# Performance work log

Measured on AMD Instinct MI355X. Metric: run time of the kernel, lower is better.

## Reference

```python
import jax, jax.numpy as jnp
import numpy as np

N_NODES = 100000


def _gcn_norm(edge_index, num_nodes):
    # PyG gcn_norm with add_self_loops=True, edge_weight=1:
    # A_hat = A + I; norm_e = deg^{-1/2}[src] * deg^{-1/2}[dst]
    loop = jnp.arange(num_nodes, dtype=edge_index.dtype)
    src = jnp.concatenate([edge_index[0], loop])
    dst = jnp.concatenate([edge_index[1], loop])
    deg = jax.ops.segment_sum(jnp.ones_like(src, dtype=jnp.float32), dst,
                              num_segments=num_nodes)
    dinv = jnp.where(deg > 0, jax.lax.rsqrt(deg), 0.0)
    norm = dinv[src] * dinv[dst]  # [E + N]
    return src, dst, norm


def _gcn_conv(x, src, dst, norm, W, b, num_nodes):
    h = x @ W                                  # [N, out] dense GEMM
    msg = h[src] * norm[:, None]               # gather + scale per edge
    out = jax.ops.segment_sum(msg, dst, num_segments=num_nodes)
    return out + b


def setup_inputs() -> dict:
    key = jax.random.key(0)
    k1, k2, k3, k4, k5, k6 = jax.random.split(key, 6)
    in_c, hid_c, out_c = 128, 128, 64
    E = 3200000
    x = jax.random.normal(k1, (N_NODES, in_c), dtype=jnp.float32)
    edge_index = jax.random.randint(k2, (2, E), 0, N_NODES, dtype=jnp.int64)
    # Glorot-style init for GCNConv linear weights, zero bias (PyG default)
    W1 = jax.random.normal(k3, (in_c, hid_c), dtype=jnp.float32) / np.sqrt(in_c)
    b1 = jnp.zeros((hid_c,), dtype=jnp.float32)
    W2 = jax.random.normal(k4, (hid_c, out_c), dtype=jnp.float32) / np.sqrt(hid_c)
    b2 = jnp.zeros((out_c,), dtype=jnp.float32)
    return {"x": x, "edge_index": edge_index, "W1": W1, "b1": b1,
            "W2": W2, "b2": b2}


def reference(x, edge_index, W1, b1, W2, b2):
    # Dropout is identity in eval mode (F.dropout(training=False)).
    src, dst, norm = _gcn_norm(edge_index, N_NODES)
    h = _gcn_conv(x, src, dst, norm, W1, b1, N_NODES)
    out = _gcn_conv(h, src, dst, norm, W2, b2, N_NODES)
    return out
```

## Files before the change

### kernel.cpp

```cpp
#include <hip/hip_runtime.h>
#include <hip/hip_fp16.h>
#include <cstdint>
#include <cstddef>


#define NB    391
#define BSH   8
#define CAPS  32
#define PBLK  512
#define OVB   64
#define CAPB  9216

typedef _Float16 half8 __attribute__((ext_vector_type(8)));
typedef float    floatx4 __attribute__((ext_vector_type(4)));
typedef unsigned uint4v  __attribute__((ext_vector_type(4)));


__global__ __launch_bounds__(256) void partition_k(
    const int* __restrict__ src, const int* __restrict__ dst,
    unsigned long long* __restrict__ ov64, int* __restrict__ ovcnt,
    unsigned* __restrict__ tailbuf, int* __restrict__ tailcnt, int E) {
    __shared__ unsigned stag[NB][CAPS + 1];
    __shared__ int scnt[NB];
    __shared__ int ovn;
    const int t = threadIdx.x, bid = blockIdx.x;
    for (int i = t; i < NB; i += 256) scnt[i] = 0;
    if (t == 0) ovn = 0;
    __syncthreads();

    const int Q = E >> 2;
    const int per = (Q + PBLK - 1) / PBLK;
    const int qbeg = bid * per;
    const int qend = min(qbeg + per, Q);
    const int4* src4 = (const int4*)src;
    const int4* dst4 = (const int4*)dst;

    for (int q = qbeg + t; q < qend; q += 256) {
        const int4 s4 = src4[q];
        const int4 d4 = dst4[q];
#pragma unroll
        for (int j = 0; j < 4; ++j) {
            const int s = (&s4.x)[j], d = (&d4.x)[j];
            const int b = d >> BSH;
            const unsigned rec = ((unsigned)(d & 255) << 17) | (unsigned)s;
            const int slot = atomicAdd(&scnt[b], 1);
            if (slot < CAPS) stag[b][slot] = rec;
            else {
                const int pos = atomicAdd(&ovn, 1);
                if (pos < OVB)
                    ov64[(size_t)bid * OVB + pos] =
                        ((unsigned long long)(unsigned)d << 17) | (unsigned)s;
            }
        }
    }
    if (bid == 0) {
        for (int e = (E & ~3) + t; e < E; e += 256) {
            const int s = src[e], d = dst[e];
            const int b = d >> BSH;
            const unsigned rec = ((unsigned)(d & 255) << 17) | (unsigned)s;
            const int slot = atomicAdd(&scnt[b], 1);
            if (slot < CAPS) stag[b][slot] = rec;
            else {
                const int pos = atomicAdd(&ovn, 1);
                if (pos < OVB)
                    ov64[(size_t)bid * OVB + pos] =
                        ((unsigned long long)(unsigned)d << 17) | (unsigned)s;
            }
        }
    }
    __syncthreads();

    for (int i = t; i < NB * CAPS; i += 256) {
        const int b = i >> 5, j = i & 31;
        if (j < min(scnt[b], CAPS))
            tailbuf[((size_t)b * PBLK + bid) * CAPS + j] = stag[b][j];
    }
    for (int b = t; b < NB; b += 256)
        tailcnt[bid * NB + b] = min(scnt[b], CAPS);
    if (t == 0) ovcnt[bid] = min(ovn, OVB);
}

__global__ __launch_bounds__(256) void build_w12_k(
    const unsigned long long* __restrict__ ov64, const int* __restrict__ ovcnt,
    const unsigned* __restrict__ tailbuf, const int* __restrict__ tailcnt,
    int* __restrict__ rbeg, int* __restrict__ rend,
    int* __restrict__ csr, float* __restrict__ dinv,
    const float* __restrict__ W1, const float* __restrict__ W2,
    const float* __restrict__ b1, _Float16* __restrict__ BhiT,
    _Float16* __restrict__ BloT, float* __restrict__ c2, int N) {
    __shared__ int tcs[PBLK];
    __shared__ int soff[PBLK];
    __shared__ int sseg[256];
    __shared__ unsigned lrec[CAPB + 64];
    __shared__ int cnt[256];
    __shared__ int scan[256];
    __shared__ int lpos[256];
    __shared__ int tcum_sh;
    __shared__ int ovn_sh;
    const int t = threadIdx.x, b = blockIdx.x;

    if (b >= NB) {
        const int bb = b - NB;
        if (bb < 32) {
            const int r = bb * 4 + (t >> 6);
            const int c = t & 63;
            float acc = 0.f;
            for (int k = 0; k < 128; ++k) acc += W1[r * 128 + k] * W2[k * 64 + c];
            const _Float16 h = (_Float16)acc;
            BhiT[c * 128 + r] = h;
            BloT[c * 128 + r] = (_Float16)(acc - (float)h);
        } else if (t < 64) {
            float acc = 0.f;
            for (int k = 0; k < 128; ++k) acc += b1[k] * W2[k * 64 + t];
            c2[t] = acc;
        }
        return;
    }

    const int n0 = b << BSH;
    const int nn = min(256, N - n0);
    const int gbase = b * CAPB;
    const size_t tb0 = (size_t)b * PBLK * CAPS;

    for (int i = t; i < PBLK; i += 256) tcs[i] = tailcnt[i * NB + b];
    cnt[t] = 0;
    if (t == 0) ovn_sh = 0;
    __syncthreads();

    const int a0 = tcs[2 * t], a1 = tcs[2 * t + 1];
    sseg[t] = a0 + a1;
    __syncthreads();
    for (int o = 1; o < 256; o <<= 1) {
        int x = (t >= o) ? sseg[t - o] : 0;
        __syncthreads(); sseg[t] += x; __syncthreads();
    }
    const int ex2 = sseg[t] - (a0 + a1);
    soff[2 * t] = ex2;
    soff[2 * t + 1] = ex2 + a0;
    if (t == 255) tcum_sh = sseg[255];
    __syncthreads();
    const int tcum = tcum_sh;

    for (int i = t; i < PBLK * CAPS; i += 256) {
        const int seg = i >> 5, j = i & 31;
        if (j < tcs[seg]) lrec[soff[seg] + j] = tailbuf[tb0 + i];
    }
    for (int blk = t; blk < PBLK; blk += 256) {
        const int c = ovcnt[blk];
        for (int i2 = 0; i2 < c; ++i2) {
            const unsigned long long r = ov64[(size_t)blk * OVB + i2];
            const int dd = (int)(r >> 17);
            if ((dd >> BSH) == b) {
                const int pos = atomicAdd(&ovn_sh, 1);
                lrec[tcum + pos] =
                    ((unsigned)(dd & 255) << 17) | (unsigned)(r & 0x1FFFFu);
            }
        }
    }
    __syncthreads();

    const int tot = tcum + ovn_sh;
    for (int i = t; i < tot; i += 256) atomicAdd(&cnt[lrec[i] >> 17], 1);
    __syncthreads();

    scan[t] = cnt[t];
    __syncthreads();
    for (int o = 1; o < 256; o <<= 1) {
        int x = (t >= o) ? scan[t - o] : 0;
        __syncthreads(); scan[t] += x; __syncthreads();
    }
    const int excl = scan[t] - cnt[t];
    lpos[t] = excl;
    if (t < nn) {
        rbeg[n0 + t] = gbase + excl;
        rend[n0 + t] = gbase + scan[t];
        dinv[n0 + t] = rsqrtf((float)(cnt[t] + 1));
    }
    __syncthreads();

    for (int i = t; i < tot; i += 256) {
        const unsigned r = lrec[i];
        const int pq = atomicAdd(&lpos[r >> 17], 1);
        csr[gbase + pq] = (int)(r & 0x1FFFFu);
    }
}

__global__ __launch_bounds__(256) void gemm_mfma_k(
    const float* __restrict__ X, const _Float16* __restrict__ BhiT,
    const _Float16* __restrict__ BloT, const float* __restrict__ dinv,
    __half* __restrict__ g, int N) {
    const int t = threadIdx.x;
    const int wave = t >> 6, lane = t & 63;
    const int m16 = lane & 15;
    const int quad = lane >> 4;
    const int rowbase = blockIdx.x * 64 + wave * 16;
    const int arow = min(rowbase + m16, N - 1);

    floatx4 acc[4] = {{0.f,0.f,0.f,0.f},{0.f,0.f,0.f,0.f},
                      {0.f,0.f,0.f,0.f},{0.f,0.f,0.f,0.f}};

#pragma unroll
    for (int ks = 0; ks < 4; ++ks) {
        const int k0 = ks * 32 + quad * 8;
        const float4 xa = *(const float4*)(X + (size_t)arow * 128 + k0);
        const float4 xb = *(const float4*)(X + (size_t)arow * 128 + k0 + 4);
        const float xs[8] = {xa.x, xa.y, xa.z, xa.w, xb.x, xb.y, xb.z, xb.w};
        half8 ahi, alo;
#pragma unroll
        for (int j = 0; j < 8; ++j) {
            const _Float16 h = (_Float16)xs[j];
            ahi[j] = h;
            alo[j] = (_Float16)(xs[j] - (float)h);
        }
#pragma unroll
        for (int c = 0; c < 4; ++c) {
            const int n = c * 16 + m16;
            const half8 bhi = *(const half8*)(BhiT + n * 128 + k0);
            const half8 blo = *(const half8*)(BloT + n * 128 + k0);
            acc[c] = __builtin_amdgcn_mfma_f32_16x16x32_f16(ahi, bhi, acc[c], 0, 0, 0);
            acc[c] = __builtin_amdgcn_mfma_f32_16x16x32_f16(ahi, blo, acc[c], 0, 0, 0);
            acc[c] = __builtin_amdgcn_mfma_f32_16x16x32_f16(alo, bhi, acc[c], 0, 0, 0);
        }
    }

#pragma unroll
    for (int r = 0; r < 4; ++r) {
        const int grow = rowbase + quad * 4 + r;
        if (grow < N) {
            const float di = dinv[grow];
#pragma unroll
            for (int c = 0; c < 4; ++c)
                g[(size_t)grow * 64 + c * 16 + m16] = __float2half(acc[c][r] * di);
        }
    }
}

template <int PASS2>
__global__ __launch_bounds__(256) void agg_k(
    const __half* __restrict__ gin, const int* __restrict__ rbeg,
    const int* __restrict__ rend, const int* __restrict__ csr,
    const float* __restrict__ dinv, void* __restrict__ outp,
    float* __restrict__ p, const float* __restrict__ c2,
    const float* __restrict__ b2, int N) {
    const int wv = (blockIdx.x * 256 + threadIdx.x) >> 6;
    const int lane = threadIdx.x & 63;
    const int half = lane >> 5;
    const int d = wv * 2 + half;
    if (d >= N) return;
    const int w    = lane & 7;
    const int slot = (lane >> 3) & 3;
    const int beg = rbeg[d], end = rend[d];
    const float di = dinv[d];
    const half8* __restrict__ grow = (const half8*)gin;

    const half8 vself = grow[((size_t)d << 3) + w];

    float acc[8];
#pragma unroll
    for (int q = 0; q < 8; ++q) acc[q] = 0.f;
    float accp = (!PASS2 && slot == 0) ? di : 0.f;

    auto accum = [&](half8 f) {
        const uint4v u = __builtin_bit_cast(uint4v, f);
#pragma unroll
        for (int q = 0; q < 4; ++q) {
            asm("v_fma_mix_f32 %0, %1, 1.0, %0 op_sel:[0,0,0] op_sel_hi:[1,0,0]"
                : "+v"(acc[2 * q]) : "v"(u[q]));
            asm("v_fma_mix_f32 %0, %1, 1.0, %0 op_sel:[1,0,0] op_sel_hi:[1,0,0]"
                : "+v"(acc[2 * q + 1]) : "v"(u[q]));
        }
    };

    int e = beg + slot;
    while (e + 12 < end) {
        const int s0 = csr[e], s1 = csr[e + 4], s2 = csr[e + 8], s3 = csr[e + 12];
        const half8 f0 = grow[((size_t)s0 << 3) + w];
        const half8 f1 = grow[((size_t)s1 << 3) + w];
        const half8 f2 = grow[((size_t)s2 << 3) + w];
        const half8 f3 = grow[((size_t)s3 << 3) + w];
        if (!PASS2) accp += dinv[s0] + dinv[s1] + dinv[s2] + dinv[s3];
        accum(f0); accum(f1); accum(f2); accum(f3);
        e += 16;
    }
    if (e + 4 < end) {
        const int s0 = csr[e], s1 = csr[e + 4];
        const half8 f0 = grow[((size_t)s0 << 3) + w];
        const half8 f1 = grow[((size_t)s1 << 3) + w];
        if (!PASS2) accp += dinv[s0] + dinv[s1];
        accum(f0); accum(f1);
        e += 8;
    }
    while (e < end) {
        const int s0 = csr[e];
        const half8 f0 = grow[((size_t)s0 << 3) + w];
        if (!PASS2) accp += dinv[s0];
        accum(f0);
        e += 4;
    }

#pragma unroll
    for (int m = 8; m <= 16; m <<= 1) {
#pragma unroll
        for (int q = 0; q < 8; ++q) acc[q] += __shfl_xor(acc[q], m);
        if (!PASS2) accp += __shfl_xor(accp, m);
    }

    if (slot == 0) {
        const __half2* sh2 = (const __half2*)&vself;
#pragma unroll
        for (int q = 0; q < 4; ++q) {
            const float2 t2 = __half22float2(sh2[q]);
            acc[2 * q]     += t2.x;
            acc[2 * q + 1] += t2.y;
        }
        if (PASS2) {
            const float pd = p[d];
            float o[8];
#pragma unroll
            for (int q = 0; q < 8; ++q)
                o[q] = acc[q] * di + pd * c2[w * 8 + q] + b2[w * 8 + q];
            float4* op = (float4*)outp + ((size_t)d << 4) + w * 2;
            op[0] = make_float4(o[0], o[1], o[2], o[3]);
            op[1] = make_float4(o[4], o[5], o[6], o[7]);
        } else {
            const float sc = di * di;
            half8 ov;
#pragma unroll
            for (int q = 0; q < 8; ++q) ov[q] = (_Float16)(acc[q] * sc);
            ((half8*)outp)[((size_t)d << 3) + w] = ov;
            if ((lane & 31) == 0) p[d] = di * accp;
        }
    }
}

extern "C" void kernel_launch(void* const* d_in, const int* in_sizes, int n_in,
                              void* d_out, int out_size, void* d_ws, size_t ws_size,
                              hipStream_t stream) {
    const float* x  = (const float*)d_in[0];
    const int*   ei = (const int*)d_in[1];
    const float* W1 = (const float*)d_in[2];
    const float* b1 = (const float*)d_in[3];
    const float* W2 = (const float*)d_in[4];
    const float* b2 = (const float*)d_in[5];
    float* out = (float*)d_out;

    const int N = in_sizes[0] / 128;
    const int E = in_sizes[1] / 2;
    const int* src = ei;
    const int* dst = ei + E;

    char* ws = (char*)d_ws;
    auto take = [&](size_t bytes) { char* q = ws; ws += (bytes + 255) & ~(size_t)255; return q; };
    int*      rbeg    = (int*)     take((size_t)N * 4);
    int*      rendp   = (int*)     take((size_t)N * 4);
    float*    dinv    = (float*)   take((size_t)N * 4);
    float*    pbuf    = (float*)   take((size_t)N * 4);
    _Float16* BhiT    = (_Float16*)take(128 * 64 * 2);
    _Float16* BloT    = (_Float16*)take(128 * 64 * 2);
    float*    c2      = (float*)   take(64 * 4);
    int*      ovcnt   = (int*)     take((size_t)PBLK * 4);
    unsigned long long* ov64 = (unsigned long long*)take((size_t)PBLK * OVB * 8);
    int*      tailcnt = (int*)     take((size_t)NB * PBLK * 4);
    unsigned* tailbuf = (unsigned*)take((size_t)NB * PBLK * CAPS * 4);
    int*      csr     = (int*)     take((size_t)NB * CAPB * 4);
    __half*   g       = (__half*)  take((size_t)N * 64 * 2);
    __half*   t1      = (__half*)  take((size_t)N * 64 * 2);

    partition_k<<<PBLK, 256, 0, stream>>>(src, dst, ov64, ovcnt, tailbuf, tailcnt, E);
    build_w12_k<<<NB + 33, 256, 0, stream>>>(ov64, ovcnt, tailbuf, tailcnt,
                                             rbeg, rendp, csr, dinv,
                                             W1, W2, b1, BhiT, BloT, c2, N);
    gemm_mfma_k<<<(N + 63) / 64, 256, 0, stream>>>(x, BhiT, BloT, dinv, g, N);

    const int aggBlocks = (N + 7) / 8;
    agg_k<0><<<aggBlocks, 256, 0, stream>>>(g,  rbeg, rendp, csr, dinv, t1,  pbuf, c2, b2, N);
    agg_k<1><<<aggBlocks, 256, 0, stream>>>(t1, rbeg, rendp, csr, dinv, out, pbuf, c2, b2, N);
}
```

Measured before the change: 298.9 us.

## Stage partitioned edges directly into CSR buckets via atomic per-bucket cursors

Partition blocks now reserve space in each destination bucket with a global atomic cursor and write their staged records straight into the CSR region, instead of a per-block padded tail buffer plus count table. The build kernel drops the 512-segment prefix scan and sparse gather and just reads a contiguous prefix of its bucket. This removes a large padded intermediate buffer and its strided traffic, at the cost of global atomics, an extra memset, and a nondeterministic edge order within each bucket.

```diff
diff --git a/kernel.cpp b/kernel.cpp
--- a/kernel.cpp
+++ b/kernel.cpp
@@ -18,10 +18,11 @@
 
 __global__ __launch_bounds__(256) void partition_k(
     const int* __restrict__ src, const int* __restrict__ dst,
-    unsigned long long* __restrict__ ov64, int* __restrict__ ovcnt,
-    unsigned* __restrict__ tailbuf, int* __restrict__ tailcnt, int E) {
+    int* __restrict__ cursor, unsigned long long* __restrict__ ov64,
+    int* __restrict__ ovcnt, int* __restrict__ csr, int E) {
     __shared__ unsigned stag[NB][CAPS + 1];
     __shared__ int scnt[NB];
+    __shared__ int sbase[NB];
     __shared__ int ovn;
     const int t = threadIdx.x, bid = blockIdx.x;
     for (int i = t; i < NB; i += 256) scnt[i] = 0;
@@ -70,32 +71,30 @@
     }
     __syncthreads();
 
+    for (int b = t; b < NB; b += 256)
+        sbase[b] = atomicAdd(&cursor[b], min(scnt[b], CAPS));
+    __syncthreads();
+
     for (int i = t; i < NB * CAPS; i += 256) {
         const int b = i >> 5, j = i & 31;
         if (j < min(scnt[b], CAPS))
-            tailbuf[((size_t)b * PBLK + bid) * CAPS + j] = stag[b][j];
-    }
-    for (int b = t; b < NB; b += 256)
-        tailcnt[bid * NB + b] = min(scnt[b], CAPS);
+            csr[(size_t)b * CAPB + sbase[b] + j] = (int)stag[b][j];
+    }
     if (t == 0) ovcnt[bid] = min(ovn, OVB);
 }
 
 __global__ __launch_bounds__(256) void build_w12_k(
+    const int* __restrict__ cursor,
     const unsigned long long* __restrict__ ov64, const int* __restrict__ ovcnt,
-    const unsigned* __restrict__ tailbuf, const int* __restrict__ tailcnt,
     int* __restrict__ rbeg, int* __restrict__ rend,
     int* __restrict__ csr, float* __restrict__ dinv,
     const float* __restrict__ W1, const float* __restrict__ W2,
     const float* __restrict__ b1, _Float16* __restrict__ BhiT,
     _Float16* __restrict__ BloT, float* __restrict__ c2, int N) {
-    __shared__ int tcs[PBLK];
-    __shared__ int soff[PBLK];
-    __shared__ int sseg[256];
     __shared__ unsigned lrec[CAPB + 64];
     __shared__ int cnt[256];
     __shared__ int scan[256];
     __shared__ int lpos[256];
-    __shared__ int tcum_sh;
     __shared__ int ovn_sh;
     const int t = threadIdx.x, b = blockIdx.x;
 
@@ -120,31 +119,13 @@
     const int n0 = b << BSH;
     const int nn = min(256, N - n0);
     const int gbase = b * CAPB;
-    const size_t tb0 = (size_t)b * PBLK * CAPS;
-
-    for (int i = t; i < PBLK; i += 256) tcs[i] = tailcnt[i * NB + b];
+    const int tstag = cursor[b];
+
     cnt[t] = 0;
     if (t == 0) ovn_sh = 0;
     __syncthreads();
 
-    const int a0 = tcs[2 * t], a1 = tcs[2 * t + 1];
-    sseg[t] = a0 + a1;
-    __syncthreads();
-    for (int o = 1; o < 256; o <<= 1) {
-        int x = (t >= o) ? sseg[t - o] : 0;
-        __syncthreads(); sseg[t] += x; __syncthreads();
-    }
-    const int ex2 = sseg[t] - (a0 + a1);
-    soff[2 * t] = ex2;
-    soff[2 * t + 1] = ex2 + a0;
-    if (t == 255) tcum_sh = sseg[255];
-    __syncthreads();
-    const int tcum = tcum_sh;
-
-    for (int i = t; i < PBLK * CAPS; i += 256) {
-        const int seg = i >> 5, j = i & 31;
-        if (j < tcs[seg]) lrec[soff[seg] + j] = tailbuf[tb0 + i];
-    }
+    for (int i = t; i < tstag; i += 256) lrec[i] = (unsigned)csr[gbase + i];
     for (int blk = t; blk < PBLK; blk += 256) {
         const int c = ovcnt[blk];
         for (int i2 = 0; i2 < c; ++i2) {
@@ -152,14 +133,14 @@
             const int dd = (int)(r >> 17);
             if ((dd >> BSH) == b) {
                 const int pos = atomicAdd(&ovn_sh, 1);
-                lrec[tcum + pos] =
+                lrec[tstag + pos] =
                     ((unsigned)(dd & 255) << 17) | (unsigned)(r & 0x1FFFFu);
             }
         }
     }
     __syncthreads();
 
-    const int tot = tcum + ovn_sh;
+    const int tot = tstag + ovn_sh;
     for (int i = t; i < tot; i += 256) atomicAdd(&cnt[lrec[i] >> 17], 1);
     __syncthreads();
 
@@ -351,6 +332,7 @@
 
     char* ws = (char*)d_ws;
     auto take = [&](size_t bytes) { char* q = ws; ws += (bytes + 255) & ~(size_t)255; return q; };
+    int*      cursor  = (int*)     take((size_t)NB * 4);
     int*      rbeg    = (int*)     take((size_t)N * 4);
     int*      rendp   = (int*)     take((size_t)N * 4);
     float*    dinv    = (float*)   take((size_t)N * 4);
@@ -360,14 +342,14 @@
     float*    c2      = (float*)   take(64 * 4);
     int*      ovcnt   = (int*)     take((size_t)PBLK * 4);
     unsigned long long* ov64 = (unsigned long long*)take((size_t)PBLK * OVB * 8);
-    int*      tailcnt = (int*)     take((size_t)NB * PBLK * 4);
-    unsigned* tailbuf = (unsigned*)take((size_t)NB * PBLK * CAPS * 4);
     int*      csr     = (int*)     take((size_t)NB * CAPB * 4);
     __half*   g       = (__half*)  take((size_t)N * 64 * 2);
     __half*   t1      = (__half*)  take((size_t)N * 64 * 2);
 
-    partition_k<<<PBLK, 256, 0, stream>>>(src, dst, ov64, ovcnt, tailbuf, tailcnt, E);
-    build_w12_k<<<NB + 33, 256, 0, stream>>>(ov64, ovcnt, tailbuf, tailcnt,
+    hipMemsetAsync(cursor, 0, (size_t)NB * 4, stream);
+
+    partition_k<<<PBLK, 256, 0, stream>>>(src, dst, cursor, ov64, ovcnt, csr, E);
+    build_w12_k<<<NB + 33, 256, 0, stream>>>(cursor, ov64, ovcnt,
                                              rbeg, rendp, csr, dinv,
                                              W1, W2, b1, BhiT, BloT, c2, N);
     gemm_mfma_k<<<(N + 63) / 64, 256, 0, stream>>>(x, BhiT, BloT, dinv, g, N);
```

After: 285.0 us. 1.05x faster.
